# Performance work log

Measured on AMD Instinct MI355X. Metric: run time of the kernel, lower is better.

The kernel has to match this reference:

```python
import jax, jax.numpy as jnp
import numpy as np

N_NODES = 50000


def _sage_conv(x, src, dst, Wl, Wr, b):
    # mean aggregation of source-node features onto targets (PyG SAGEConv, aggr='mean')
    msg = x[src]                                              # [E, d]
    agg = jax.ops.segment_sum(msg, dst, num_segments=N_NODES)  # [N, d]
    cnt = jax.ops.segment_sum(jnp.ones((src.shape[0],), x.dtype), dst, num_segments=N_NODES)
    mean = agg / jnp.maximum(cnt, 1.0)[:, None]
    return mean @ Wl + x @ Wr + b


def _layer_norm(x, g, b, eps=1e-5):
    mu = jnp.mean(x, axis=-1, keepdims=True)
    var = jnp.var(x, axis=-1, keepdims=True)
    return (x - mu) * jax.lax.rsqrt(var + eps) * g + b


def setup_inputs() -> dict:
    key = jax.random.key(0)
    ks = jax.random.split(key, 10)
    d_in, d_h, d_out = 128, 128, 2
    scale_h = 1.0 / np.sqrt(d_in)
    x = jax.random.normal(ks[0], (N_NODES, d_in), jnp.float32)
    edge_index = jax.random.randint(ks[1], (2, 800000), 0, N_NODES, dtype=jnp.int64)
    return {
        "x": x,
        "edge_index": edge_index,
        "W1l": jax.random.normal(ks[2], (d_in, d_h), jnp.float32) * scale_h,
        "W1r": jax.random.normal(ks[3], (d_in, d_h), jnp.float32) * scale_h,
        "b1": jnp.zeros((d_h,), jnp.float32),
        "ln1_g": jnp.ones((d_h,), jnp.float32),
        "ln1_b": jnp.zeros((d_h,), jnp.float32),
        "W2l": jax.random.normal(ks[4], (d_h, d_h), jnp.float32) * scale_h,
        "W2r": jax.random.normal(ks[5], (d_h, d_h), jnp.float32) * scale_h,
        "b2": jnp.zeros((d_h,), jnp.float32),
        "ln2_g": jnp.ones((d_h,), jnp.float32),
        "ln2_b": jnp.zeros((d_h,), jnp.float32),
        "W3l": jax.random.normal(ks[6], (d_h, d_out), jnp.float32) * scale_h,
        "W3r": jax.random.normal(ks[7], (d_h, d_out), jnp.float32) * scale_h,
        "b3": jnp.zeros((d_out,), jnp.float32),
    }


def reference(x, edge_index, W1l, W1r, b1, ln1_g, ln1_b, W2l, W2r, b2, ln2_g, ln2_b, W3l, W3r, b3):
    src, dst = edge_index[0], edge_index[1]
    h = _sage_conv(x, src, dst, W1l, W1r, b1)
    h = jax.nn.relu(_layer_norm(h, ln1_g, ln1_b))
    h = _sage_conv(h, src, dst, W2l, W2r, b2)
    h = jax.nn.relu(_layer_norm(h, ln2_g, ln2_b))
    return _sage_conv(h, src, dst, W3l, W3r, b3)
```

## Files before the change

kernel.cpp:

```cpp
#include <hip/hip_runtime.h>

#define N_NODES 50000
#define CAP 64
#define NBK 196
#define BCAP2 4608
#define EPB 4096
#define PB ((int)0xAAAAAAAA)

typedef unsigned int uint;
typedef unsigned short ushort;
typedef __attribute__((ext_vector_type(8))) short bf16x8;
typedef __attribute__((ext_vector_type(4))) float f32x4;

__device__ inline float bf2f(uint u) { u <<= 16; return __builtin_bit_cast(float, u); }
__device__ inline ushort f2bf(float f) {
    uint u = __builtin_bit_cast(uint, f);
    u = (u + 0x7fffu + ((u >> 16) & 1u)) >> 16;
    return (ushort)u;
}


__global__ __launch_bounds__(256) void k_prep(
    const int* __restrict__ src, const int* __restrict__ dst, int E,
    int* __restrict__ bcnt, uint* __restrict__ bstage,
    const float* __restrict__ x, ushort* __restrict__ Xb, int n4,
    const float* __restrict__ W1l, const float* __restrict__ W1r, ushort* __restrict__ Wp1,
    const float* __restrict__ W2l, const float* __restrict__ W2r, ushort* __restrict__ Wp2,
    int bBin, int bC) {
    __shared__ uint recs[EPB];
    __shared__ int hist[NBK], base[NBK], cursor[NBK], gbase[NBK];
    __shared__ int ws[4];
    int b = blockIdx.x, t = threadIdx.x;
    if (b < bBin) {
        int i0 = b * EPB;
        for (int i = t; i < NBK; i += 256) hist[i] = 0;
        __syncthreads();
        uint r[16];
#pragma unroll
        for (int k = 0; k < 16; ++k) {
            int i = i0 + k * 256 + t;
            if (i < E) {
                int s = src[i], d = dst[i];
                r[k] = ((uint)s << 16) | (uint)d;
                atomicAdd(&hist[d >> 8], 1);
            } else r[k] = 0xffffffffu;
        }
        __syncthreads();
        int lane = t & 63, w = t >> 6;
        int v = (t < NBK) ? hist[t] : 0;
        int xsc = v;
#pragma unroll
        for (int o = 1; o < 64; o <<= 1) {
            int y = __shfl_up(xsc, o, 64);
            if (lane >= o) xsc += y;
        }
        if (lane == 63) ws[w] = xsc;
        __syncthreads();
        int add = 0;
        for (int k = 0; k < 4; ++k)
            if (k < w) add += ws[k];
        if (t < NBK) { base[t] = xsc - v + add; cursor[t] = xsc - v + add; }
        __syncthreads();
#pragma unroll
        for (int k = 0; k < 16; ++k) {
            if (r[k] != 0xffffffffu) {
                int bk = (int)((r[k] & 0xffffu) >> 8);
                int pos = atomicAdd(&cursor[bk], 1);
                recs[pos] = r[k];
            }
        }
        __syncthreads();
        for (int i = t; i < NBK; i += 256) {
            int h = hist[i];
            gbase[i] = h ? (atomicAdd(&bcnt[i], h) - PB) : 0;
        }
        __syncthreads();
        int mblk = min(E - i0, EPB);
        for (int i = t; i < mblk; i += 256) {
            uint rr = recs[i];
            int bk = (int)((rr & 0xffffu) >> 8);
            int pos = gbase[bk] + (i - base[bk]);
            if (pos < BCAP2) bstage[(size_t)bk * BCAP2 + pos] = rr;
        }
    } else if (b < bBin + bC) {
        int i = (b - bBin) * 256 + t;
        if (i < n4) {
            float4 v = ((const float4*)x)[i];
            ushort4 o;
            o.x = f2bf(v.x); o.y = f2bf(v.y); o.z = f2bf(v.z); o.w = f2bf(v.w);
            ((ushort4*)Xb)[i] = o;
        }
    } else if (b < bBin + bC + 128) {
        int idx = (b - bBin - bC) * 256 + t;
        int k = idx >> 7, n = idx & 127;
        float v = (k < 128) ? W1l[k * 128 + n] : W1r[(k - 128) * 128 + n];
        Wp1[((k >> 3) << 10) + (n << 3) + (k & 7)] = f2bf(v);
    } else {
        int idx = (b - bBin - bC - 128) * 256 + t;
        int k = idx >> 7, n = idx & 127;
        float v = (k < 128) ? W2l[k * 128 + n] : W2r[(k - 128) * 128 + n];
        Wp2[((k >> 3) << 10) + (n << 3) + (k & 7)] = f2bf(v);
    }
}


__global__ __launch_bounds__(256) void k_csr_build(const int* __restrict__ bcnt,
                                                   const uint* __restrict__ bstage,
                                                   int* __restrict__ cnt,
                                                   ushort* __restrict__ csr, int N) {
    __shared__ int lcnt[256];
    __shared__ ushort lcsr[256 * CAP];
    int b = blockIdx.x, t = threadIdx.x;
    lcnt[t] = 0;
    __syncthreads();
    int m = min(bcnt[b] - PB, BCAP2);
    const uint* st = bstage + (size_t)b * BCAP2;
    for (int i = t; i < m; i += 256) {
        uint rr = st[i];
        int local = rr & 255;
        int slot = atomicAdd(&lcnt[local], 1);
        if (slot < CAP) lcsr[local * CAP + slot] = (ushort)(rr >> 16);
    }
    __syncthreads();
    uint4* d4 = (uint4*)(csr + (size_t)b * 256 * CAP);
    const uint4* s4 = (const uint4*)lcsr;
    for (int i = t; i < 256 * CAP * 2 / 16; i += 256) d4[i] = s4[i];
    int node = b * 256 + t;
    if (node < N) cnt[node] = min(lcnt[t], CAP);
}


__global__ __launch_bounds__(256) void k_agg(const ushort* __restrict__ X,
                                             const int* __restrict__ cnt,
                                             const ushort* __restrict__ csr,
                                             ushort* __restrict__ M, int N) {
    int node = blockIdx.x * 4 + (threadIdx.x >> 6);
    int lane = threadIdx.x & 63;
    int l = lane & 15, es = lane >> 4;
    if (node >= N) return;
    int end = cnt[node];
    const ushort* row = csr + (size_t)node * CAP;
    float a0 = 0.f, a1 = 0.f, a2 = 0.f, a3 = 0.f;
    float a4 = 0.f, a5 = 0.f, a6 = 0.f, a7 = 0.f;
    int e = 0;
    for (; e + 7 < end; e += 8) {
        int s0 = row[e + es];
        int s1 = row[e + 4 + es];
        uint4 v0 = *(const uint4*)(X + (size_t)s0 * 128 + l * 8);
        uint4 v1 = *(const uint4*)(X + (size_t)s1 * 128 + l * 8);
        a0 += bf2f(v0.x & 0xffffu) + bf2f(v1.x & 0xffffu);
        a1 += bf2f(v0.x >> 16) + bf2f(v1.x >> 16);
        a2 += bf2f(v0.y & 0xffffu) + bf2f(v1.y & 0xffffu);
        a3 += bf2f(v0.y >> 16) + bf2f(v1.y >> 16);
        a4 += bf2f(v0.z & 0xffffu) + bf2f(v1.z & 0xffffu);
        a5 += bf2f(v0.z >> 16) + bf2f(v1.z >> 16);
        a6 += bf2f(v0.w & 0xffffu) + bf2f(v1.w & 0xffffu);
        a7 += bf2f(v0.w >> 16) + bf2f(v1.w >> 16);
    }
    for (; e < end; e += 4) {
        int idx = e + es;
        if (idx < end) {
            uint4 v = *(const uint4*)(X + (size_t)row[idx] * 128 + l * 8);
            a0 += bf2f(v.x & 0xffffu); a1 += bf2f(v.x >> 16);
            a2 += bf2f(v.y & 0xffffu); a3 += bf2f(v.y >> 16);
            a4 += bf2f(v.z & 0xffffu); a5 += bf2f(v.z >> 16);
            a6 += bf2f(v.w & 0xffffu); a7 += bf2f(v.w >> 16);
        }
    }
    a0 += __shfl_xor(a0, 16); a1 += __shfl_xor(a1, 16);
    a2 += __shfl_xor(a2, 16); a3 += __shfl_xor(a3, 16);
    a4 += __shfl_xor(a4, 16); a5 += __shfl_xor(a5, 16);
    a6 += __shfl_xor(a6, 16); a7 += __shfl_xor(a7, 16);
    a0 += __shfl_xor(a0, 32); a1 += __shfl_xor(a1, 32);
    a2 += __shfl_xor(a2, 32); a3 += __shfl_xor(a3, 32);
    a4 += __shfl_xor(a4, 32); a5 += __shfl_xor(a5, 32);
    a6 += __shfl_xor(a6, 32); a7 += __shfl_xor(a7, 32);
    if (es == 0) {
        float inv = 1.0f / (float)max(end, 1);
        uint4 o;
        o.x = (uint)f2bf(a0 * inv) | ((uint)f2bf(a1 * inv) << 16);
        o.y = (uint)f2bf(a2 * inv) | ((uint)f2bf(a3 * inv) << 16);
        o.z = (uint)f2bf(a4 * inv) | ((uint)f2bf(a5 * inv) << 16);
        o.w = (uint)f2bf(a6 * inv) | ((uint)f2bf(a7 * inv) << 16);
        *(uint4*)(M + (size_t)node * 128 + l * 8) = o;
    }
}


__global__ __launch_bounds__(256, 2) void k_gemm_ln_relu(
    const ushort* __restrict__ Mb, const ushort* __restrict__ Xb,
    const ushort* __restrict__ Wp, const float* __restrict__ bias,
    const float* __restrict__ g, const float* __restrict__ bb,
    ushort* __restrict__ H, int N,
    const float* __restrict__ W3l, const float* __restrict__ W3r,
    const float* __restrict__ b3, float* __restrict__ tb, float* __restrict__ rb) {
    __shared__ ushort sW[256 * 128];
    int tid = threadIdx.x;
    int wave = tid >> 6, lane = tid & 63;
    int l15 = lane & 15, q = lane >> 4;
    int rowBase = blockIdx.x * 64 + wave * 16;
    int arow = rowBase + l15;
    if (arow >= N) arow = N - 1;

    {
        const uint4* wsrc = (const uint4*)Wp;
        uint4* wdst = (uint4*)sW;
#pragma unroll
        for (int i = 0; i < 16; ++i) wdst[i * 256 + tid] = wsrc[i * 256 + tid];
    }

    f32x4 acc[8];
#pragma unroll
    for (int t = 0; t < 8; ++t) acc[t] = (f32x4){0.f, 0.f, 0.f, 0.f};

    const ushort* aM = Mb + (size_t)arow * 128 + q * 8;
    const ushort* aX = Xb + (size_t)arow * 128 + q * 8;
    __syncthreads();
    const ushort* wq = sW + q * 1024 + l15 * 8;

#pragma unroll
    for (int s = 0; s < 8; ++s) {
        bf16x8 a = (s < 4) ? *(const bf16x8*)(aM + s * 32)
                           : *(const bf16x8*)(aX + (s - 4) * 32);
        const ushort* wbase = wq + s * 4096;
#pragma unroll
        for (int t = 0; t < 8; ++t) {
            bf16x8 b = *(const bf16x8*)(wbase + t * 128);
            acc[t] = __builtin_amdgcn_mfma_f32_16x16x32_bf16(a, b, acc[t], 0, 0, 0);
        }
    }

    const bool doProj = (tb != nullptr);
    float gj[8], bbj[8], bj[8];
    float wl0[8], wl1[8], wr0[8], wr1[8];
#pragma unroll
    for (int t = 0; t < 8; ++t) {
        int col = t * 16 + l15;
        gj[t] = g[col]; bbj[t] = bb[col]; bj[t] = bias[col];
    }
    if (doProj) {
#pragma unroll
        for (int t = 0; t < 8; ++t) {
            int col = t * 16 + l15;
            float2 a = *(const float2*)(W3l + col * 2);
            float2 c2 = *(const float2*)(W3r + col * 2);
            wl0[t] = a.x; wl1[t] = a.y; wr0[t] = c2.x; wr1[t] = c2.y;
        }
    }

#pragma unroll
    for (int r = 0; r < 4; ++r) {
        float c[8];
        float s = 0.f, ss = 0.f;
#pragma unroll
        for (int t = 0; t < 8; ++t) {
            c[t] = acc[t][r] + bj[t];
            s += c[t];
            ss += c[t] * c[t];
        }
        s += __shfl_xor(s, 1); ss += __shfl_xor(ss, 1);
        s += __shfl_xor(s, 2); ss += __shfl_xor(ss, 2);
        s += __shfl_xor(s, 4); ss += __shfl_xor(ss, 4);
        s += __shfl_xor(s, 8); ss += __shfl_xor(ss, 8);
        float mu = s * (1.0f / 128.0f);
        float var = ss * (1.0f / 128.0f) - mu * mu;
        float rsig = rsqrtf(var + 1e-5f);
        int node = rowBase + q * 4 + r;
        float y[8];
#pragma unroll
        for (int t = 0; t < 8; ++t) {
            float v = (c[t] - mu) * rsig * gj[t] + bbj[t];
            y[t] = fmaxf(v, 0.f);
        }
        if (!doProj) {
            if (node < N) {
                ushort* hp = H + (size_t)node * 128;
#pragma unroll
                for (int t = 0; t < 8; ++t) hp[t * 16 + l15] = f2bf(y[t]);
            }
        } else {
            float t0 = 0.f, t1 = 0.f, r0 = 0.f, r1 = 0.f;
#pragma unroll
            for (int t = 0; t < 8; ++t) {
                t0 += y[t] * wl0[t];
                t1 += y[t] * wl1[t];
                r0 += y[t] * wr0[t];
                r1 += y[t] * wr1[t];
            }
#pragma unroll
            for (int o = 1; o < 16; o <<= 1) {
                t0 += __shfl_xor(t0, o);
                t1 += __shfl_xor(t1, o);
                r0 += __shfl_xor(r0, o);
                r1 += __shfl_xor(r1, o);
            }
            if (l15 == 0 && node < N) {
                tb[node * 2 + 0] = t0;
                tb[node * 2 + 1] = t1;
                rb[node * 2 + 0] = r0 + b3[0];
                rb[node * 2 + 1] = r1 + b3[1];
            }
        }
    }
}


__global__ __launch_bounds__(256) void k_final(const float* __restrict__ t, const float* __restrict__ r,
                                               const int* __restrict__ cnt, const ushort* __restrict__ csr,
                                               float* __restrict__ out, int N) {
    int n = blockIdx.x * blockDim.x + threadIdx.x;
    if (n >= N) return;
    int end = cnt[n];
    const ushort* row = csr + (size_t)n * CAP;
    float a0 = 0.f, a1 = 0.f, b0 = 0.f, b1 = 0.f;
    int e = 0;
    for (; e + 3 < end; e += 4) {
        float2 v0 = *(const float2*)(t + row[e] * 2);
        float2 v1 = *(const float2*)(t + row[e + 1] * 2);
        float2 v2 = *(const float2*)(t + row[e + 2] * 2);
        float2 v3 = *(const float2*)(t + row[e + 3] * 2);
        a0 += v0.x + v1.x; a1 += v0.y + v1.y;
        b0 += v2.x + v3.x; b1 += v2.y + v3.y;
    }
    for (; e < end; ++e) {
        float2 v = *(const float2*)(t + row[e] * 2);
        a0 += v.x; a1 += v.y;
    }
    a0 += b0; a1 += b1;
    float inv = 1.0f / (float)max(end, 1);
    out[n * 2 + 0] = a0 * inv + r[n * 2 + 0];
    out[n * 2 + 1] = a1 * inv + r[n * 2 + 1];
}


extern "C" void kernel_launch(void* const* d_in, const int* in_sizes, int n_in,
                              void* d_out, int out_size, void* d_ws, size_t ws_size,
                              hipStream_t stream) {
    const float* x   = (const float*)d_in[0];
    const int* eidx  = (const int*)d_in[1];
    const float* W1l = (const float*)d_in[2];
    const float* W1r = (const float*)d_in[3];
    const float* b1  = (const float*)d_in[4];
    const float* g1  = (const float*)d_in[5];
    const float* bb1 = (const float*)d_in[6];
    const float* W2l = (const float*)d_in[7];
    const float* W2r = (const float*)d_in[8];
    const float* b2  = (const float*)d_in[9];
    const float* g2  = (const float*)d_in[10];
    const float* bb2 = (const float*)d_in[11];
    const float* W3l = (const float*)d_in[12];
    const float* W3r = (const float*)d_in[13];
    const float* b3  = (const float*)d_in[14];
    float* out = (float*)d_out;

    const int N = N_NODES;
    const int E = in_sizes[1] / 2;
    const int* src = eidx;
    const int* dst = eidx + E;

    char* ws = (char*)d_ws;
    size_t off = 0;
    auto alloc = [&](size_t bytes) -> char* {
        char* p = ws + off;
        off += (bytes + 255) & ~(size_t)255;
        return p;
    };
    int* bcnt    = (int*)alloc((size_t)NBK * sizeof(int));
    uint* bstage = (uint*)alloc((size_t)NBK * BCAP2 * sizeof(uint));
    int* cnt     = (int*)alloc((size_t)N * sizeof(int));
    ushort* csr  = (ushort*)alloc((size_t)NBK * 256 * CAP * sizeof(ushort));
    ushort* Xb   = (ushort*)alloc((size_t)N * 128 * sizeof(ushort));
    ushort* Mb   = (ushort*)alloc((size_t)N * 128 * sizeof(ushort));
    ushort* Hb   = (ushort*)alloc((size_t)N * 128 * sizeof(ushort));
    ushort* Wp1  = (ushort*)alloc((size_t)256 * 128 * sizeof(ushort));
    ushort* Wp2  = (ushort*)alloc((size_t)256 * 128 * sizeof(ushort));
    float* tbuf  = (float*)alloc((size_t)N * 2 * sizeof(float));
    float* rbuf  = (float*)alloc((size_t)N * 2 * sizeof(float));

    const int n4 = N * 128 / 4;
    const int bBin = (E + EPB - 1) / EPB;
    const int bC = (n4 + 255) / 256;

    k_prep<<<bBin + bC + 256, 256, 0, stream>>>(src, dst, E, bcnt, bstage, x, Xb, n4,
                                                W1l, W1r, Wp1, W2l, W2r, Wp2, bBin, bC);
    k_csr_build<<<NBK, 256, 0, stream>>>(bcnt, bstage, cnt, csr, N);

    k_agg<<<(N + 3) / 4, 256, 0, stream>>>(Xb, cnt, csr, Mb, N);
    k_gemm_ln_relu<<<(N + 63) / 64, 256, 0, stream>>>(Mb, Xb, Wp1, b1, g1, bb1, Hb, N,
                                                      nullptr, nullptr, nullptr, nullptr, nullptr);
    k_agg<<<(N + 3) / 4, 256, 0, stream>>>(Hb, cnt, csr, Mb, N);
    k_gemm_ln_relu<<<(N + 63) / 64, 256, 0, stream>>>(Mb, Hb, Wp2, b2, g2, bb2, nullptr, N,
                                                      W3l, W3r, b3, tbuf, rbuf);
    k_final<<<(N + 255) / 256, 256, 0, stream>>>(tbuf, rbuf, cnt, csr, out, N);
}
```

Baseline: 214.5 us.

## Store node features in four 32-column slices and aggregate per slice

Feature matrices (Xb, Mb, Hb) are stored as four column slices of 32 bf16 values per node rather than 128-wide rows. The aggregation kernel now handles one slice per block, with 16 nodes per wave and 4 lanes per node, looping to the wave's maximum degree. The intent is to shrink the working set each gather touches so it stays in L2/MALL, and to spread neighbour-index loads across lanes. In exchange, the CSR index list is read four times, divergence grows with uneven degrees, and GEMM row loads become strided across slices.

```diff
diff --git a/kernel.cpp b/kernel.cpp
--- a/kernel.cpp
+++ b/kernel.cpp
@@ -7,6 +7,8 @@
 #define EPB 4096
 #define PB ((int)0xAAAAAAAA)
 
+#define SLS ((size_t)N_NODES * 32)
+
 typedef unsigned int uint;
 typedef unsigned short ushort;
 typedef __attribute__((ext_vector_type(8))) short bf16x8;
@@ -23,7 +25,7 @@
 __global__ __launch_bounds__(256) void k_prep(
     const int* __restrict__ src, const int* __restrict__ dst, int E,
     int* __restrict__ bcnt, uint* __restrict__ bstage,
-    const float* __restrict__ x, ushort* __restrict__ Xb, int n4,
+    const float* __restrict__ x, ushort* __restrict__ Xb, int n8,
     const float* __restrict__ W1l, const float* __restrict__ W1r, ushort* __restrict__ Wp1,
     const float* __restrict__ W2l, const float* __restrict__ W2r, ushort* __restrict__ Wp2,
     int bBin, int bC) {
@@ -84,11 +86,16 @@
         }
     } else if (b < bBin + bC) {
         int i = (b - bBin) * 256 + t;
-        if (i < n4) {
-            float4 v = ((const float4*)x)[i];
-            ushort4 o;
-            o.x = f2bf(v.x); o.y = f2bf(v.y); o.z = f2bf(v.z); o.w = f2bf(v.w);
-            ((ushort4*)Xb)[i] = o;
+        if (i < n8) {
+            int node = i >> 4, f8 = i & 15;
+            const float4* xp = (const float4*)(x + (size_t)node * 128 + f8 * 8);
+            float4 v0 = xp[0], v1 = xp[1];
+            uint4 o;
+            o.x = (uint)f2bf(v0.x) | ((uint)f2bf(v0.y) << 16);
+            o.y = (uint)f2bf(v0.z) | ((uint)f2bf(v0.w) << 16);
+            o.z = (uint)f2bf(v1.x) | ((uint)f2bf(v1.y) << 16);
+            o.w = (uint)f2bf(v1.z) | ((uint)f2bf(v1.w) << 16);
+            *(uint4*)(Xb + (size_t)(f8 >> 2) * SLS + (size_t)node * 32 + (f8 & 3) * 8) = o;
         }
     } else if (b < bBin + bC + 128) {
         int idx = (b - bBin - bC) * 256 + t;
@@ -134,55 +141,40 @@
                                              const int* __restrict__ cnt,
                                              const ushort* __restrict__ csr,
                                              ushort* __restrict__ M, int N) {
-    int node = blockIdx.x * 4 + (threadIdx.x >> 6);
-    int lane = threadIdx.x & 63;
-    int l = lane & 15, es = lane >> 4;
-    if (node >= N) return;
-    int end = cnt[node];
-    const ushort* row = csr + (size_t)node * CAP;
+    int slice = blockIdx.x & 3;
+    int nb = blockIdx.x >> 2;
+    int lane = threadIdx.x & 63, wave = threadIdx.x >> 6;
+    int es = lane >> 2, fl = lane & 3;
+    int node = nb * 64 + wave * 16 + es;
+    int end = (node < N) ? cnt[node] : 0;
+    int md = end;
+    md = max(md, __shfl_xor(md, 4));
+    md = max(md, __shfl_xor(md, 8));
+    md = max(md, __shfl_xor(md, 16));
+    md = max(md, __shfl_xor(md, 32));
+    const ushort* rp = csr + (size_t)node * CAP;
+    const ushort* Xs = X + (size_t)slice * SLS + fl * 8;
     float a0 = 0.f, a1 = 0.f, a2 = 0.f, a3 = 0.f;
     float a4 = 0.f, a5 = 0.f, a6 = 0.f, a7 = 0.f;
-    int e = 0;
-    for (; e + 7 < end; e += 8) {
-        int s0 = row[e + es];
-        int s1 = row[e + 4 + es];
-        uint4 v0 = *(const uint4*)(X + (size_t)s0 * 128 + l * 8);
-        uint4 v1 = *(const uint4*)(X + (size_t)s1 * 128 + l * 8);
-        a0 += bf2f(v0.x & 0xffffu) + bf2f(v1.x & 0xffffu);
-        a1 += bf2f(v0.x >> 16) + bf2f(v1.x >> 16);
-        a2 += bf2f(v0.y & 0xffffu) + bf2f(v1.y & 0xffffu);
-        a3 += bf2f(v0.y >> 16) + bf2f(v1.y >> 16);
-        a4 += bf2f(v0.z & 0xffffu) + bf2f(v1.z & 0xffffu);
-        a5 += bf2f(v0.z >> 16) + bf2f(v1.z >> 16);
-        a6 += bf2f(v0.w & 0xffffu) + bf2f(v1.w & 0xffffu);
-        a7 += bf2f(v0.w >> 16) + bf2f(v1.w >> 16);
-    }
-    for (; e < end; e += 4) {
-        int idx = e + es;
-        if (idx < end) {
-            uint4 v = *(const uint4*)(X + (size_t)row[idx] * 128 + l * 8);
-            a0 += bf2f(v.x & 0xffffu); a1 += bf2f(v.x >> 16);
-            a2 += bf2f(v.y & 0xffffu); a3 += bf2f(v.y >> 16);
-            a4 += bf2f(v.z & 0xffffu); a5 += bf2f(v.z >> 16);
-            a6 += bf2f(v.w & 0xffffu); a7 += bf2f(v.w >> 16);
-        }
-    }
-    a0 += __shfl_xor(a0, 16); a1 += __shfl_xor(a1, 16);
-    a2 += __shfl_xor(a2, 16); a3 += __shfl_xor(a3, 16);
-    a4 += __shfl_xor(a4, 16); a5 += __shfl_xor(a5, 16);
-    a6 += __shfl_xor(a6, 16); a7 += __shfl_xor(a7, 16);
-    a0 += __shfl_xor(a0, 32); a1 += __shfl_xor(a1, 32);
-    a2 += __shfl_xor(a2, 32); a3 += __shfl_xor(a3, 32);
-    a4 += __shfl_xor(a4, 32); a5 += __shfl_xor(a5, 32);
-    a6 += __shfl_xor(a6, 32); a7 += __shfl_xor(a7, 32);
-    if (es == 0) {
+#pragma unroll 4
+    for (int e = 0; e < md; ++e) {
+        if (e < end) {
+            int s = rp[e];
+            uint4 v = *(const uint4*)(Xs + (size_t)s * 32);
+            a0 += bf2f(v.x); a1 += bf2f(v.x >> 16);
+            a2 += bf2f(v.y); a3 += bf2f(v.y >> 16);
+            a4 += bf2f(v.z); a5 += bf2f(v.z >> 16);
+            a6 += bf2f(v.w); a7 += bf2f(v.w >> 16);
+        }
+    }
+    if (node < N) {
         float inv = 1.0f / (float)max(end, 1);
         uint4 o;
         o.x = (uint)f2bf(a0 * inv) | ((uint)f2bf(a1 * inv) << 16);
         o.y = (uint)f2bf(a2 * inv) | ((uint)f2bf(a3 * inv) << 16);
         o.z = (uint)f2bf(a4 * inv) | ((uint)f2bf(a5 * inv) << 16);
         o.w = (uint)f2bf(a6 * inv) | ((uint)f2bf(a7 * inv) << 16);
-        *(uint4*)(M + (size_t)node * 128 + l * 8) = o;
+        *(uint4*)(M + (size_t)slice * SLS + (size_t)node * 32 + fl * 8) = o;
     }
 }
 
@@ -213,15 +205,15 @@
 #pragma unroll
     for (int t = 0; t < 8; ++t) acc[t] = (f32x4){0.f, 0.f, 0.f, 0.f};
 
-    const ushort* aM = Mb + (size_t)arow * 128 + q * 8;
-    const ushort* aX = Xb + (size_t)arow * 128 + q * 8;
+    const ushort* aM = Mb + (size_t)arow * 32 + q * 8;
+    const ushort* aX = Xb + (size_t)arow * 32 + q * 8;
     __syncthreads();
     const ushort* wq = sW + q * 1024 + l15 * 8;
 
 #pragma unroll
     for (int s = 0; s < 8; ++s) {
-        bf16x8 a = (s < 4) ? *(const bf16x8*)(aM + s * 32)
-                           : *(const bf16x8*)(aX + (s - 4) * 32);
+        bf16x8 a = (s < 4) ? *(const bf16x8*)(aM + (size_t)s * SLS)
+                           : *(const bf16x8*)(aX + (size_t)(s - 4) * SLS);
         const ushort* wbase = wq + s * 4096;
 #pragma unroll
         for (int t = 0; t < 8; ++t) {
@@ -274,9 +266,10 @@
         }
         if (!doProj) {
             if (node < N) {
-                ushort* hp = H + (size_t)node * 128;
-#pragma unroll
-                for (int t = 0; t < 8; ++t) hp[t * 16 + l15] = f2bf(y[t]);
+                ushort* hp = H + (size_t)node * 32;
+#pragma unroll
+                for (int t = 0; t < 8; ++t)
+                    hp[(size_t)(t >> 1) * SLS + (t & 1) * 16 + l15] = f2bf(y[t]);
             }
         } else {
             float t0 = 0.f, t1 = 0.f, r0 = 0.f, r1 = 0.f;
@@ -377,18 +370,19 @@
     float* tbuf  = (float*)alloc((size_t)N * 2 * sizeof(float));
     float* rbuf  = (float*)alloc((size_t)N * 2 * sizeof(float));
 
-    const int n4 = N * 128 / 4;
+    const int n8 = N * 16;
     const int bBin = (E + EPB - 1) / EPB;
-    const int bC = (n4 + 255) / 256;
-
-    k_prep<<<bBin + bC + 256, 256, 0, stream>>>(src, dst, E, bcnt, bstage, x, Xb, n4,
+    const int bC = (n8 + 255) / 256;
+
+    k_prep<<<bBin + bC + 256, 256, 0, stream>>>(src, dst, E, bcnt, bstage, x, Xb, n8,
                                                 W1l, W1r, Wp1, W2l, W2r, Wp2, bBin, bC);
     k_csr_build<<<NBK, 256, 0, stream>>>(bcnt, bstage, cnt, csr, N);
 
-    k_agg<<<(N + 3) / 4, 256, 0, stream>>>(Xb, cnt, csr, Mb, N);
+    const int aggGrid = 4 * ((N + 63) / 64);
+    k_agg<<<aggGrid, 256, 0, stream>>>(Xb, cnt, csr, Mb, N);
     k_gemm_ln_relu<<<(N + 63) / 64, 256, 0, stream>>>(Mb, Xb, Wp1, b1, g1, bb1, Hb, N,
                                                       nullptr, nullptr, nullptr, nullptr, nullptr);
-    k_agg<<<(N + 3) / 4, 256, 0, stream>>>(Hb, cnt, csr, Mb, N);
+    k_agg<<<aggGrid, 256, 0, stream>>>(Hb, cnt, csr, Mb, N);
     k_gemm_ln_relu<<<(N + 63) / 64, 256, 0, stream>>>(Mb, Hb, Wp2, b2, g2, bb2, nullptr, N,
                                                       W3l, W3r, b3, tbuf, rbuf);
     k_final<<<(N + 255) / 256, 256, 0, stream>>>(tbuf, rbuf, cnt, csr, out, N);
```

Result: slower. 251.9 us (+17.4%).

## Fuse neighbor mean aggregation into GEMM+LayerNorm layer kernel via shared memory

Applied to the files above, without the earlier changes.

Merges the separate aggregation kernel and the GEMM/LayerNorm/ReLU kernel into one per-layer kernel. Each 64-node block stages its CSR rows in shared memory, computes the mean-aggregated rows into a shared tile, then reuses the same shared buffer for the weight matrix and runs the MFMA GEMM from shared memory. This removes the global round trip of the aggregated matrix and two kernel launches. In exchange, the gather phase now runs with only 782 blocks of 4 waves, each wave handling 16 nodes serially, so latency hiding for the random gathers may be worse.

```diff
diff --git a/kernel.cpp b/kernel.cpp
--- a/kernel.cpp
+++ b/kernel.cpp
@@ -6,6 +6,7 @@
 #define BCAP2 4608
 #define EPB 4096
 #define PB ((int)0xAAAAAAAA)
+#define RS 72
 
 typedef unsigned int uint;
 typedef unsigned short ushort;
@@ -130,103 +131,114 @@
 }
 
 
-__global__ __launch_bounds__(256) void k_agg(const ushort* __restrict__ X,
-                                             const int* __restrict__ cnt,
-                                             const ushort* __restrict__ csr,
-                                             ushort* __restrict__ M, int N) {
-    int node = blockIdx.x * 4 + (threadIdx.x >> 6);
-    int lane = threadIdx.x & 63;
-    int l = lane & 15, es = lane >> 4;
-    if (node >= N) return;
-    int end = cnt[node];
-    const ushort* row = csr + (size_t)node * CAP;
-    float a0 = 0.f, a1 = 0.f, a2 = 0.f, a3 = 0.f;
-    float a4 = 0.f, a5 = 0.f, a6 = 0.f, a7 = 0.f;
-    int e = 0;
-    for (; e + 7 < end; e += 8) {
-        int s0 = row[e + es];
-        int s1 = row[e + 4 + es];
-        uint4 v0 = *(const uint4*)(X + (size_t)s0 * 128 + l * 8);
-        uint4 v1 = *(const uint4*)(X + (size_t)s1 * 128 + l * 8);
-        a0 += bf2f(v0.x & 0xffffu) + bf2f(v1.x & 0xffffu);
-        a1 += bf2f(v0.x >> 16) + bf2f(v1.x >> 16);
-        a2 += bf2f(v0.y & 0xffffu) + bf2f(v1.y & 0xffffu);
-        a3 += bf2f(v0.y >> 16) + bf2f(v1.y >> 16);
-        a4 += bf2f(v0.z & 0xffffu) + bf2f(v1.z & 0xffffu);
-        a5 += bf2f(v0.z >> 16) + bf2f(v1.z >> 16);
-        a6 += bf2f(v0.w & 0xffffu) + bf2f(v1.w & 0xffffu);
-        a7 += bf2f(v0.w >> 16) + bf2f(v1.w >> 16);
-    }
-    for (; e < end; e += 4) {
-        int idx = e + es;
-        if (idx < end) {
-            uint4 v = *(const uint4*)(X + (size_t)row[idx] * 128 + l * 8);
-            a0 += bf2f(v.x & 0xffffu); a1 += bf2f(v.x >> 16);
-            a2 += bf2f(v.y & 0xffffu); a3 += bf2f(v.y >> 16);
-            a4 += bf2f(v.z & 0xffffu); a5 += bf2f(v.z >> 16);
-            a6 += bf2f(v.w & 0xffffu); a7 += bf2f(v.w >> 16);
-        }
-    }
-    a0 += __shfl_xor(a0, 16); a1 += __shfl_xor(a1, 16);
-    a2 += __shfl_xor(a2, 16); a3 += __shfl_xor(a3, 16);
-    a4 += __shfl_xor(a4, 16); a5 += __shfl_xor(a5, 16);
-    a6 += __shfl_xor(a6, 16); a7 += __shfl_xor(a7, 16);
-    a0 += __shfl_xor(a0, 32); a1 += __shfl_xor(a1, 32);
-    a2 += __shfl_xor(a2, 32); a3 += __shfl_xor(a3, 32);
-    a4 += __shfl_xor(a4, 32); a5 += __shfl_xor(a5, 32);
-    a6 += __shfl_xor(a6, 32); a7 += __shfl_xor(a7, 32);
-    if (es == 0) {
-        float inv = 1.0f / (float)max(end, 1);
-        uint4 o;
-        o.x = (uint)f2bf(a0 * inv) | ((uint)f2bf(a1 * inv) << 16);
-        o.y = (uint)f2bf(a2 * inv) | ((uint)f2bf(a3 * inv) << 16);
-        o.z = (uint)f2bf(a4 * inv) | ((uint)f2bf(a5 * inv) << 16);
-        o.w = (uint)f2bf(a6 * inv) | ((uint)f2bf(a7 * inv) << 16);
-        *(uint4*)(M + (size_t)node * 128 + l * 8) = o;
-    }
-}
-
-
-__global__ __launch_bounds__(256, 2) void k_gemm_ln_relu(
-    const ushort* __restrict__ Mb, const ushort* __restrict__ Xb,
-    const ushort* __restrict__ Wp, const float* __restrict__ bias,
-    const float* __restrict__ g, const float* __restrict__ bb,
-    ushort* __restrict__ H, int N,
+__global__ __launch_bounds__(256, 2) void k_layer(
+    const ushort* __restrict__ X, const int* __restrict__ cnt,
+    const ushort* __restrict__ csr, const ushort* __restrict__ Wp,
+    const float* __restrict__ bias, const float* __restrict__ g,
+    const float* __restrict__ bb, ushort* __restrict__ H, int N,
     const float* __restrict__ W3l, const float* __restrict__ W3r,
     const float* __restrict__ b3, float* __restrict__ tb, float* __restrict__ rb) {
-    __shared__ ushort sW[256 * 128];
-    int tid = threadIdx.x;
-    int wave = tid >> 6, lane = tid & 63;
-    int l15 = lane & 15, q = lane >> 4;
-    int rowBase = blockIdx.x * 64 + wave * 16;
-    int arow = rowBase + l15;
-    if (arow >= N) arow = N - 1;
+    __shared__ __align__(16) char uraw[256 * 128 * 2];
+    ushort* srow = (ushort*)uraw;
+    int* scnt = (int*)(uraw + 64 * RS * 2);
+    ushort* sW = (ushort*)uraw;
+    __shared__ ushort sM[64 * 128];
+    int t = threadIdx.x;
+    int node0 = blockIdx.x * 64;
+
+    {
+        int ln = t >> 2, c = t & 3;
+        const uint4* s = (const uint4*)(csr + (size_t)(node0 + ln) * CAP + c * 16);
+        uint4* d = (uint4*)(srow + ln * RS + c * 16);
+        d[0] = s[0];
+        d[1] = s[1];
+        if (t < 64) scnt[t] = (node0 + t < N) ? cnt[node0 + t] : 0;
+    }
+    __syncthreads();
+
+    int wave = t >> 6, lane = t & 63;
+    int l = lane & 15, es = lane >> 4;
+
+    for (int k = 0; k < 16; ++k) {
+        int ln = wave * 16 + k;
+        int end = scnt[ln];
+        const ushort* rp = srow + ln * RS;
+        float a0 = 0.f, a1 = 0.f, a2 = 0.f, a3 = 0.f;
+        float a4 = 0.f, a5 = 0.f, a6 = 0.f, a7 = 0.f;
+        int e = 0;
+        for (; e + 7 < end; e += 8) {
+            int s0 = rp[e + es];
+            int s1 = rp[e + 4 + es];
+            uint4 v0 = *(const uint4*)(X + (size_t)s0 * 128 + l * 8);
+            uint4 v1 = *(const uint4*)(X + (size_t)s1 * 128 + l * 8);
+            a0 += bf2f(v0.x & 0xffffu) + bf2f(v1.x & 0xffffu);
+            a1 += bf2f(v0.x >> 16) + bf2f(v1.x >> 16);
+            a2 += bf2f(v0.y & 0xffffu) + bf2f(v1.y & 0xffffu);
+            a3 += bf2f(v0.y >> 16) + bf2f(v1.y >> 16);
+            a4 += bf2f(v0.z & 0xffffu) + bf2f(v1.z & 0xffffu);
+            a5 += bf2f(v0.z >> 16) + bf2f(v1.z >> 16);
+            a6 += bf2f(v0.w & 0xffffu) + bf2f(v1.w & 0xffffu);
+            a7 += bf2f(v0.w >> 16) + bf2f(v1.w >> 16);
+        }
+        for (; e < end; e += 4) {
+            int idx = e + es;
+            if (idx < end) {
+                uint4 v = *(const uint4*)(X + (size_t)rp[idx] * 128 + l * 8);
+                a0 += bf2f(v.x & 0xffffu); a1 += bf2f(v.x >> 16);
+                a2 += bf2f(v.y & 0xffffu); a3 += bf2f(v.y >> 16);
+                a4 += bf2f(v.z & 0xffffu); a5 += bf2f(v.z >> 16);
+                a6 += bf2f(v.w & 0xffffu); a7 += bf2f(v.w >> 16);
+            }
+        }
+        a0 += __shfl_xor(a0, 16); a1 += __shfl_xor(a1, 16);
+        a2 += __shfl_xor(a2, 16); a3 += __shfl_xor(a3, 16);
+        a4 += __shfl_xor(a4, 16); a5 += __shfl_xor(a5, 16);
+        a6 += __shfl_xor(a6, 16); a7 += __shfl_xor(a7, 16);
+        a0 += __shfl_xor(a0, 32); a1 += __shfl_xor(a1, 32);
+        a2 += __shfl_xor(a2, 32); a3 += __shfl_xor(a3, 32);
+        a4 += __shfl_xor(a4, 32); a5 += __shfl_xor(a5, 32);
+        a6 += __shfl_xor(a6, 32); a7 += __shfl_xor(a7, 32);
+        if (es == 0) {
+            float inv = 1.0f / (float)max(end, 1);
+            uint4 o;
+            o.x = (uint)f2bf(a0 * inv) | ((uint)f2bf(a1 * inv) << 16);
+            o.y = (uint)f2bf(a2 * inv) | ((uint)f2bf(a3 * inv) << 16);
+            o.z = (uint)f2bf(a4 * inv) | ((uint)f2bf(a5 * inv) << 16);
+            o.w = (uint)f2bf(a6 * inv) | ((uint)f2bf(a7 * inv) << 16);
+            *(uint4*)(sM + ln * 128 + l * 8) = o;
+        }
+    }
+    __syncthreads();
 
     {
         const uint4* wsrc = (const uint4*)Wp;
         uint4* wdst = (uint4*)sW;
 #pragma unroll
-        for (int i = 0; i < 16; ++i) wdst[i * 256 + tid] = wsrc[i * 256 + tid];
-    }
+        for (int i = 0; i < 16; ++i) wdst[i * 256 + t] = wsrc[i * 256 + t];
+    }
+    __syncthreads();
+
+    int l15 = lane & 15, q = lane >> 4;
+    int rowBase = node0 + wave * 16;
+    int arow = rowBase + l15;
+    if (arow >= N) arow = N - 1;
+    const ushort* aM = sM + (wave * 16 + l15) * 128 + q * 8;
+    const ushort* aX = X + (size_t)arow * 128 + q * 8;
+    const ushort* wq = sW + q * 1024 + l15 * 8;
 
     f32x4 acc[8];
 #pragma unroll
-    for (int t = 0; t < 8; ++t) acc[t] = (f32x4){0.f, 0.f, 0.f, 0.f};
-
-    const ushort* aM = Mb + (size_t)arow * 128 + q * 8;
-    const ushort* aX = Xb + (size_t)arow * 128 + q * 8;
-    __syncthreads();
-    const ushort* wq = sW + q * 1024 + l15 * 8;
+    for (int k = 0; k < 8; ++k) acc[k] = (f32x4){0.f, 0.f, 0.f, 0.f};
 
 #pragma unroll
     for (int s = 0; s < 8; ++s) {
-        bf16x8 a = (s < 4) ? *(const bf16x8*)(aM + s * 32)
-                           : *(const bf16x8*)(aX + (s - 4) * 32);
+        bf16x8 av = (s < 4) ? *(const bf16x8*)(aM + s * 32)
+                            : *(const bf16x8*)(aX + (s - 4) * 32);
         const ushort* wbase = wq + s * 4096;
 #pragma unroll
-        for (int t = 0; t < 8; ++t) {
-            bf16x8 b = *(const bf16x8*)(wbase + t * 128);
-            acc[t] = __builtin_amdgcn_mfma_f32_16x16x32_bf16(a, b, acc[t], 0, 0, 0);
+        for (int k = 0; k < 8; ++k) {
+            bf16x8 bv = *(const bf16x8*)(wbase + k * 128);
+            acc[k] = __builtin_amdgcn_mfma_f32_16x16x32_bf16(av, bv, acc[k], 0, 0, 0);
         }
     }
 
@@ -234,58 +246,58 @@
     float gj[8], bbj[8], bj[8];
     float wl0[8], wl1[8], wr0[8], wr1[8];
 #pragma unroll
-    for (int t = 0; t < 8; ++t) {
-        int col = t * 16 + l15;
-        gj[t] = g[col]; bbj[t] = bb[col]; bj[t] = bias[col];
+    for (int k = 0; k < 8; ++k) {
+        int col = k * 16 + l15;
+        gj[k] = g[col]; bbj[k] = bb[col]; bj[k] = bias[col];
     }
     if (doProj) {
 #pragma unroll
-        for (int t = 0; t < 8; ++t) {
-            int col = t * 16 + l15;
-            float2 a = *(const float2*)(W3l + col * 2);
-            float2 c2 = *(const float2*)(W3r + col * 2);
-            wl0[t] = a.x; wl1[t] = a.y; wr0[t] = c2.x; wr1[t] = c2.y;
+        for (int k = 0; k < 8; ++k) {
+            int col = k * 16 + l15;
+            float2 aa = *(const float2*)(W3l + col * 2);
+            float2 cc = *(const float2*)(W3r + col * 2);
+            wl0[k] = aa.x; wl1[k] = aa.y; wr0[k] = cc.x; wr1[k] = cc.y;
         }
     }
 
 #pragma unroll
     for (int r = 0; r < 4; ++r) {
         float c[8];
-        float s = 0.f, ss = 0.f;
-#pragma unroll
-        for (int t = 0; t < 8; ++t) {
-            c[t] = acc[t][r] + bj[t];
-            s += c[t];
-            ss += c[t] * c[t];
-        }
-        s += __shfl_xor(s, 1); ss += __shfl_xor(ss, 1);
-        s += __shfl_xor(s, 2); ss += __shfl_xor(ss, 2);
-        s += __shfl_xor(s, 4); ss += __shfl_xor(ss, 4);
-        s += __shfl_xor(s, 8); ss += __shfl_xor(ss, 8);
-        float mu = s * (1.0f / 128.0f);
+        float s1 = 0.f, ss = 0.f;
+#pragma unroll
+        for (int k = 0; k < 8; ++k) {
+            c[k] = acc[k][r] + bj[k];
+            s1 += c[k];
+            ss += c[k] * c[k];
+        }
+        s1 += __shfl_xor(s1, 1); ss += __shfl_xor(ss, 1);
+        s1 += __shfl_xor(s1, 2); ss += __shfl_xor(ss, 2);
+        s1 += __shfl_xor(s1, 4); ss += __shfl_xor(ss, 4);
+        s1 += __shfl_xor(s1, 8); ss += __shfl_xor(ss, 8);
+        float mu = s1 * (1.0f / 128.0f);
         float var = ss * (1.0f / 128.0f) - mu * mu;
         float rsig = rsqrtf(var + 1e-5f);
         int node = rowBase + q * 4 + r;
         float y[8];
 #pragma unroll
-        for (int t = 0; t < 8; ++t) {
-            float v = (c[t] - mu) * rsig * gj[t] + bbj[t];
-            y[t] = fmaxf(v, 0.f);
+        for (int k = 0; k < 8; ++k) {
+            float v = (c[k] - mu) * rsig * gj[k] + bbj[k];
+            y[k] = fmaxf(v, 0.f);
         }
         if (!doProj) {
             if (node < N) {
                 ushort* hp = H + (size_t)node * 128;
 #pragma unroll
-                for (int t = 0; t < 8; ++t) hp[t * 16 + l15] = f2bf(y[t]);
+                for (int k = 0; k < 8; ++k) hp[k * 16 + l15] = f2bf(y[k]);
             }
         } else {
             float t0 = 0.f, t1 = 0.f, r0 = 0.f, r1 = 0.f;
 #pragma unroll
-            for (int t = 0; t < 8; ++t) {
-                t0 += y[t] * wl0[t];
-                t1 += y[t] * wl1[t];
-                r0 += y[t] * wr0[t];
-                r1 += y[t] * wr1[t];
+            for (int k = 0; k < 8; ++k) {
+                t0 += y[k] * wl0[k];
+                t1 += y[k] * wl1[k];
+                r0 += y[k] * wr0[k];
+                r1 += y[k] * wr1[k];
             }
 #pragma unroll
             for (int o = 1; o < 16; o <<= 1) {
@@ -370,7 +382,6 @@
     int* cnt     = (int*)alloc((size_t)N * sizeof(int));
     ushort* csr  = (ushort*)alloc((size_t)NBK * 256 * CAP * sizeof(ushort));
     ushort* Xb   = (ushort*)alloc((size_t)N * 128 * sizeof(ushort));
-    ushort* Mb   = (ushort*)alloc((size_t)N * 128 * sizeof(ushort));
     ushort* Hb   = (ushort*)alloc((size_t)N * 128 * sizeof(ushort));
     ushort* Wp1  = (ushort*)alloc((size_t)256 * 128 * sizeof(ushort));
     ushort* Wp2  = (ushort*)alloc((size_t)256 * 128 * sizeof(ushort));
@@ -380,16 +391,15 @@
     const int n4 = N * 128 / 4;
     const int bBin = (E + EPB - 1) / EPB;
     const int bC = (n4 + 255) / 256;
+    const int nLayerBlk = (N + 63) / 64;
 
     k_prep<<<bBin + bC + 256, 256, 0, stream>>>(src, dst, E, bcnt, bstage, x, Xb, n4,
                                                 W1l, W1r, Wp1, W2l, W2r, Wp2, bBin, bC);
     k_csr_build<<<NBK, 256, 0, stream>>>(bcnt, bstage, cnt, csr, N);
 
-    k_agg<<<(N + 3) / 4, 256, 0, stream>>>(Xb, cnt, csr, Mb, N);
-    k_gemm_ln_relu<<<(N + 63) / 64, 256, 0, stream>>>(Mb, Xb, Wp1, b1, g1, bb1, Hb, N,
-                                                      nullptr, nullptr, nullptr, nullptr, nullptr);
-    k_agg<<<(N + 3) / 4, 256, 0, stream>>>(Hb, cnt, csr, Mb, N);
-    k_gemm_ln_relu<<<(N + 63) / 64, 256, 0, stream>>>(Mb, Hb, Wp2, b2, g2, bb2, nullptr, N,
-                                                      W3l, W3r, b3, tbuf, rbuf);
+    k_layer<<<nLayerBlk, 256, 0, stream>>>(Xb, cnt, csr, Wp1, b1, g1, bb1, Hb, N,
+                                           nullptr, nullptr, nullptr, nullptr, nullptr);
+    k_layer<<<nLayerBlk, 256, 0, stream>>>(Hb, cnt, csr, Wp2, b2, g2, bb2, nullptr, N,
+                                           W3l, W3r, b3, tbuf, rbuf);
     k_final<<<(N + 255) / 256, 256, 0, stream>>>(tbuf, rbuf, cnt, csr, out, N);
 }
```

Measured after the change: 249.7 us. 1.16x slower.
